# Kernel tuning notes

Measured on AMD Instinct MI355X. Metric: run time of the kernel, lower is better.

Reference implementation:

```python
import jax, jax.numpy as jnp
import numpy as np

# Static sensor configuration (from init_kwargs)
WIDTH = 1024
HEIGHT = 1024
X0, Y0 = -1.0, -1.0
DX = (1.0 - (-1.0)) / WIDTH
DY = (1.0 - (-1.0)) / HEIGHT
SIGMA = 0.1
KERNEL_SIZE = 2

_off = np.arange(-KERNEL_SIZE, KERNEL_SIZE + 1)
_ox, _oy = np.meshgrid(_off, _off, indexing='xy')
OFF_X = jnp.asarray(_ox.flatten(), dtype=jnp.int32)  # [(2k+1)^2] = [25]
OFF_Y = jnp.asarray(_oy.flatten(), dtype=jnp.int32)

N_POINTS = 2_000_000


def setup_inputs() -> dict:
    key = jax.random.key(0)
    k1, k2, k3 = jax.random.split(key, 3)
    x = jax.random.uniform(k1, (N_POINTS,), dtype=jnp.float32)       # in [0,1) subset of bounds
    y = jax.random.uniform(k2, (N_POINTS,), dtype=jnp.float32)
    values = jax.random.normal(k3, (N_POINTS,), dtype=jnp.float32)
    return {"x": x, "y": y, "values": values}


def reference(x, y, values):
    # Map to pixel coordinates
    x_pix = (x - X0) / DX
    y_pix = (y - Y0) / DY
    xi_base = jnp.floor(x_pix).astype(jnp.int32)
    yi_base = jnp.floor(y_pix).astype(jnp.int32)
    x_frac = x_pix - xi_base
    y_frac = y_pix - yi_base

    # [N, 25] neighbor pixel indices and Gaussian weights
    xi = xi_base[:, None] + OFF_X[None, :]
    yi = yi_base[:, None] + OFF_Y[None, :]
    dist_x = x_frac[:, None] - OFF_X[None, :].astype(x_frac.dtype)
    dist_y = y_frac[:, None] - OFF_Y[None, :].astype(y_frac.dtype)
    weights = jnp.exp(-0.5 * (dist_x ** 2 + dist_y ** 2) / (SIGMA ** 2))
    weights = weights / jnp.sum(weights, axis=1, keepdims=True)

    valid = (xi >= 0) & (xi < WIDTH) & (yi >= 0) & (yi < HEIGHT)
    xi = jnp.clip(xi, 0, WIDTH - 1)
    yi = jnp.clip(yi, 0, HEIGHT - 1)

    splatted = values[:, None] * weights * valid  # [N, 25]
    flat_idx = (yi * WIDTH + xi).reshape(-1)      # [N*25]
    img_flat = jax.ops.segment_sum(splatted.reshape(-1), flat_idx,
                                   num_segments=HEIGHT * WIDTH)
    return img_flat.reshape(HEIGHT, WIDTH)
```

## Files before the change

kernel.cpp:

```cpp
#include <hip/hip_runtime.h>
#include <hip/hip_bf16.h>

#define WIDTH 1024
#define HEIGHT 1024
#define IMG_ELEMS (WIDTH * HEIGHT)
#define TPX 32
#define NTILES (TPX * TPX)
#define NB 256
#define BT 1024
#define CAPR 80
#define CAPP 36
#define PTS_CAP 8448

#define OFF_PTS   0
#define OFF_BIDX  (OFF_PTS + 2 * PTS_CAP)
#define OFF_HCNT  (OFF_BIDX + (NTILES * CAPP) / 2)
#define OFF_RCNT  (OFF_HCNT + NTILES)
#define OFF_RDST  (OFF_RCNT + NB)
#define OFF_STMP  (OFF_RDST + NB)
#define SMEM_U32  (OFF_STMP + NB)


__device__ __forceinline__ void point_geom(float px, float py, int& cxb, int& cyb,
                                           float& ax, float& ay) {
    float xp = (px + 1.0f) * 512.0f;
    float yp = (py + 1.0f) * 512.0f;
    int xb = (int)floorf(xp);
    int yb = (int)floorf(yp);
    float xf = xp - (float)xb;
    float yf = yp - (float)yb;
    ax = 1.0f / (1.0f + __expf(100.0f * xf - 50.0f));
    ay = 1.0f / (1.0f + __expf(100.0f * yf - 50.0f));
    cxb = min(max(xb, 0), WIDTH - 1);
    cyb = min(max(yb, 0), HEIGHT - 1);
}

__device__ __forceinline__ void splat_one(float px, float py, float val,
                                          unsigned* cursor, uint2* payload,
                                          unsigned bbase) {
    int cxb, cyb; float ax, ay;
    point_geom(px, py, cxb, cyb, ax, ay);
    int tile = (cyb >> 5) * TPX + (cxb >> 5);
    unsigned pos = atomicAdd(&cursor[tile], 1u);
    if (pos < CAPR) {
        unsigned axq = (unsigned)(ax * 2047.0f + 0.5f);
        unsigned ayq = (unsigned)(ay * 2047.0f + 0.5f);
        unsigned packed = axq | (ayq << 11) |
                          ((unsigned)(cxb & 31) << 22) | ((unsigned)(cyb & 31) << 27);
        payload[(size_t)(bbase | (unsigned)tile) * CAPR + pos] =
            make_uint2(__float_as_uint(val), packed);
    }
}

__global__ void __launch_bounds__(BT)
k_sortlocal(const float* __restrict__ x, const float* __restrict__ y,
            const float* __restrict__ v, uint2* __restrict__ payload,
            unsigned* __restrict__ runCnt, float4* __restrict__ outv,
            int n, int ppb) {
    __shared__ unsigned cursor[NTILES];
    int b = blockIdx.x;
    cursor[threadIdx.x] = 0u;
    outv[(unsigned)b * 1024u + threadIdx.x] = make_float4(0.f, 0.f, 0.f, 0.f);
    __syncthreads();
    int lo = b * ppb;
    int hi = min(n, lo + ppb);
    unsigned bbase = (unsigned)(b << 10);
    for (int base = lo + (int)threadIdx.x * 4; base < hi; base += BT * 4) {
        if (base + 3 < hi) {
            float4 x4 = *(const float4*)&x[base];
            float4 y4 = *(const float4*)&y[base];
            float4 v4 = *(const float4*)&v[base];
            splat_one(x4.x, y4.x, v4.x, cursor, payload, bbase);
            splat_one(x4.y, y4.y, v4.y, cursor, payload, bbase);
            splat_one(x4.z, y4.z, v4.z, cursor, payload, bbase);
            splat_one(x4.w, y4.w, v4.w, cursor, payload, bbase);
        } else {
            for (int i = base; i < hi; ++i)
                splat_one(x[i], y[i], v[i], cursor, payload, bbase);
        }
    }
    __syncthreads();
    runCnt[(unsigned)b * NTILES + threadIdx.x] = min(cursor[threadIdx.x], (unsigned)CAPR);
}

__global__ void __launch_bounds__(BT)
k_accum(const uint2* __restrict__ payload, const unsigned* __restrict__ runCnt,
        float* __restrict__ out) {
    __shared__ unsigned smem[SMEM_U32];
    uint2*          pts  = (uint2*)&smem[OFF_PTS];
    unsigned short* bidx = (unsigned short*)&smem[OFF_BIDX];
    unsigned*       hcnt = &smem[OFF_HCNT];
    unsigned*       rcnt = &smem[OFF_RCNT];
    unsigned*       rdst = &smem[OFF_RDST];
    unsigned*       stmp = &smem[OFF_STMP];
    float*          exT01 = (float*)&smem[OFF_PTS];
    float*          exT11 = (float*)&smem[OFF_PTS + BT];

    unsigned b = blockIdx.x;
    unsigned t;
    if (b < 256u) {
        t = (16u + (b >> 4)) * 32u + 16u + (b & 15u);
    } else {
        unsigned r = b - 256u;
        if (r < 512u) t = r;
        else { unsigned q = r - 512u; t = (16u + (q >> 4)) * 32u + (q & 15u); }
    }

    int p = threadIdx.x;
    unsigned lane = p & 63, w = p >> 6;
    unsigned c0 = 0u;
    if (p < NB) { c0 = runCnt[(unsigned)p * NTILES + t]; rcnt[p] = c0; }
    hcnt[p] = 0u;
    unsigned tsum = c0;
#pragma unroll
    for (int d = 32; d >= 1; d >>= 1) tsum += __shfl_down(tsum, d, 64);
    if (p < NB && lane == 0) rdst[w] = tsum;
    __syncthreads();
    unsigned total = rdst[0] + rdst[1] + rdst[2] + rdst[3];
    if (total == 0) return;

    unsigned vsc = c0;
#pragma unroll
    for (int d = 1; d < 64; d <<= 1) {
        unsigned tmp = __shfl_up(vsc, d, 64);
        if (lane >= (unsigned)d) vsc += tmp;
    }
    __syncthreads();
    if (p < NB && lane == 63) stmp[w] = vsc;
    __syncthreads();
    if (p == 0) {
        unsigned a = 0;
#pragma unroll
        for (int k = 0; k < 4; ++k) { unsigned tt = stmp[k]; stmp[k] = a; a += tt; }
    }
    __syncthreads();
    if (p < NB) rdst[p] = vsc - c0 + stmp[w];
    __syncthreads();

    for (int k = 0; k < 16; ++k) {
        int r = (int)w * 16 + k;
        unsigned cnt = rcnt[r], dst = rdst[r];
        const unsigned long long* g =
            (const unsigned long long*)(payload + (size_t)((unsigned)(r << 10) | t) * CAPR);
        for (unsigned j = lane; j < cnt; j += 64) {
            unsigned long long raw = __builtin_nontemporal_load(&g[j]);
            uint2 pl = make_uint2((unsigned)raw, (unsigned)(raw >> 32));
            unsigned slot = dst + j;
            if (slot < PTS_CAP) {
                pts[slot] = pl;
                unsigned pix = (pl.y >> 22) & 1023u;
                unsigned pos = atomicAdd(&hcnt[pix], 1u);
                if (pos < CAPP) bidx[pix * CAPP + pos] = (unsigned short)slot;
            }
        }
    }
    __syncthreads();

    float t00 = 0.0f, t10 = 0.0f, t01 = 0.0f, t11 = 0.0f;
    unsigned cnt = min(hcnt[p], (unsigned)CAPP);
    for (unsigned e = 0; e < cnt; ++e) {
        uint2 sp = pts[bidx[p * CAPP + e]];
        float val = __uint_as_float(sp.x);
        float ax = (float)(sp.y & 2047u) * (1.0f / 2047.0f);
        float ay = (float)((sp.y >> 11) & 2047u) * (1.0f / 2047.0f);
        float bx = 1.0f - ax, by = 1.0f - ay;
        t00 += val * ax * ay;
        t10 += val * bx * ay;
        t01 += val * ax * by;
        t11 += val * bx * by;
    }
    __syncthreads();
    exT01[p] = t01;
    exT11[p] = t11;
    __syncthreads();

    int lx = p & 31, ly = p >> 5;
    int gx = (int)((t & 31u) << 5) + lx;
    int gy = (int)((t >> 5) << 5) + ly;
    size_t g = (size_t)gy * WIDTH + gx;
    float t10l = __shfl_up(t10, 1, 64);
    float sum = t00;
    if (lx > 0) sum += t10l;
    if (ly > 0) sum += exT01[p - 32];
    if (lx > 0 && ly > 0) sum += exT11[p - 33];
    if (lx == 0 || ly == 0) atomicAdd(&out[g], sum);
    else out[g] = sum;

    bool xr = (gx + 1 < WIDTH), yd = (gy + 1 < HEIGHT);
    if (lx == 31 && xr) {
        atomicAdd(&out[g + 1], t10);
        if (yd) atomicAdd(&out[g + WIDTH + 1], t11);
    }
    if (ly == 31 && yd) {
        atomicAdd(&out[g + WIDTH], t01);
        if (lx < 31 && xr) atomicAdd(&out[g + WIDTH + 1], t11);
    }
}

__global__ void __launch_bounds__(256)
splat_direct(const float* __restrict__ x, const float* __restrict__ y,
             const float* __restrict__ v, float* __restrict__ out, int n) {
    int i = blockIdx.x * blockDim.x + threadIdx.x;
    if (i >= n) return;
    int cxb, cyb; float ax, ay;
    point_geom(x[i], y[i], cxb, cyb, ax, ay);
    float val = v[i];
    float bx = 1.0f - ax, by = 1.0f - ay;
    float* row = out + cyb * WIDTH;
    atomicAdd(row + cxb, val * ax * ay);
    if (cxb + 1 < WIDTH) atomicAdd(row + cxb + 1, val * bx * ay);
    if (cyb + 1 < HEIGHT) {
        row += WIDTH;
        atomicAdd(row + cxb, val * ax * by);
        if (cxb + 1 < WIDTH) atomicAdd(row + cxb + 1, val * bx * by);
    }
}

extern "C" void kernel_launch(void* const* d_in, const int* in_sizes, int n_in,
                              void* d_out, int out_size, void* d_ws, size_t ws_size,
                              hipStream_t stream) {
    const float* x = (const float*)d_in[0];
    const float* y = (const float*)d_in[1];
    const float* v = (const float*)d_in[2];
    float* out = (float*)d_out;
    int n = in_sizes[0];
    int ppb = ((n + NB - 1) / NB + 7) & ~7;

    size_t off_payload = 0;
    size_t off_runcnt  = off_payload + (size_t)NB * NTILES * CAPR * sizeof(uint2);
    size_t need        = off_runcnt + (size_t)NB * NTILES * sizeof(unsigned);
    bool caps_ok = (ppb <= 8192) && (out_size == IMG_ELEMS);

    if (ws_size >= need && caps_ok) {
        char* ws = (char*)d_ws;
        uint2*    payload = (uint2*)(ws + off_payload);
        unsigned* runCnt  = (unsigned*)(ws + off_runcnt);

        k_sortlocal<<<NB, BT, 0, stream>>>(x, y, v, payload, runCnt,
                                           (float4*)out, n, ppb);
        k_accum<<<NTILES, BT, 0, stream>>>(payload, runCnt, out);
    } else {
        (void)hipMemsetAsync(out, 0, (size_t)out_size * sizeof(float), stream);
        splat_direct<<<(n + 255) / 256, 256, 0, stream>>>(x, y, v, out, n);
    }
}
```

Before: 101.2 us.

## Stage bucketed payload in LDS and write compact per-block runs coalesced

The binning kernel no longer scatters each point straight to a fixed-capacity global slot per (block, tile). Each block now counting-sorts its points into shared memory, computing per-tile offsets with a block-wide scan, and writes the packed sorted buffer to global memory with coalesced 16-byte stores. It stores offset and count together in runCnt, and the accumulation kernel reads runs at those offsets using 8 lanes per run. This removes scattered 8-byte global writes and shrinks the payload footprint. It assumes at most 8 points per thread (ppb ≤ 8192), drops the per-tile capacity clamp, and uses 64KB+ of LDS per block.

```diff
diff --git a/kernel.cpp b/kernel.cpp
--- a/kernel.cpp
+++ b/kernel.cpp
@@ -8,7 +8,7 @@
 #define NTILES (TPX * TPX)
 #define NB 256
 #define BT 1024
-#define CAPR 80
+#define BSTRIDE 8192
 #define CAPP 36
 #define PTS_CAP 8448
 
@@ -17,7 +17,8 @@
 #define OFF_HCNT  (OFF_BIDX + (NTILES * CAPP) / 2)
 #define OFF_RCNT  (OFF_HCNT + NTILES)
 #define OFF_RDST  (OFF_RCNT + NB)
-#define OFF_STMP  (OFF_RDST + NB)
+#define OFF_ROFF  (OFF_RDST + NB)
+#define OFF_STMP  (OFF_ROFF + NB)
 #define SMEM_U32  (OFF_STMP + NB)
 
 
@@ -35,52 +36,95 @@
     cyb = min(max(yb, 0), HEIGHT - 1);
 }
 
-__device__ __forceinline__ void splat_one(float px, float py, float val,
-                                          unsigned* cursor, uint2* payload,
-                                          unsigned bbase) {
-    int cxb, cyb; float ax, ay;
-    point_geom(px, py, cxb, cyb, ax, ay);
-    int tile = (cyb >> 5) * TPX + (cxb >> 5);
-    unsigned pos = atomicAdd(&cursor[tile], 1u);
-    if (pos < CAPR) {
-        unsigned axq = (unsigned)(ax * 2047.0f + 0.5f);
-        unsigned ayq = (unsigned)(ay * 2047.0f + 0.5f);
-        unsigned packed = axq | (ayq << 11) |
-                          ((unsigned)(cxb & 31) << 22) | ((unsigned)(cyb & 31) << 27);
-        payload[(size_t)(bbase | (unsigned)tile) * CAPR + pos] =
-            make_uint2(__float_as_uint(val), packed);
-    }
-}
-
 __global__ void __launch_bounds__(BT)
 k_sortlocal(const float* __restrict__ x, const float* __restrict__ y,
             const float* __restrict__ v, uint2* __restrict__ payload,
             unsigned* __restrict__ runCnt, float4* __restrict__ outv,
             int n, int ppb) {
     __shared__ unsigned cursor[NTILES];
+    __shared__ unsigned wtot[BT / 64];
+    __shared__ __align__(16) uint2 stage[BSTRIDE];
+
     int b = blockIdx.x;
-    cursor[threadIdx.x] = 0u;
-    outv[(unsigned)b * 1024u + threadIdx.x] = make_float4(0.f, 0.f, 0.f, 0.f);
-    __syncthreads();
+    int p = threadIdx.x;
+    cursor[p] = 0u;
+    outv[(unsigned)b * 1024u + p] = make_float4(0.f, 0.f, 0.f, 0.f);
+    __syncthreads();
+
     int lo = b * ppb;
     int hi = min(n, lo + ppb);
-    unsigned bbase = (unsigned)(b << 10);
-    for (int base = lo + (int)threadIdx.x * 4; base < hi; base += BT * 4) {
+
+    uint2 pay[8];
+    unsigned meta[8];
+
+    auto enc = [&](int s, float px, float py, float pv) {
+        int cxb, cyb; float ax, ay;
+        point_geom(px, py, cxb, cyb, ax, ay);
+        unsigned tile = (unsigned)((cyb >> 5) * TPX + (cxb >> 5));
+        unsigned pos = atomicAdd(&cursor[tile], 1u);
+        unsigned axq = (unsigned)(ax * 2047.0f + 0.5f);
+        unsigned ayq = (unsigned)(ay * 2047.0f + 0.5f);
+        pay[s] = make_uint2(__float_as_uint(pv),
+                            axq | (ayq << 11) | ((unsigned)(cxb & 31) << 22) |
+                            ((unsigned)(cyb & 31) << 27));
+        meta[s] = (tile << 16) | pos;
+    };
+
+#pragma unroll
+    for (int it = 0; it < 2; ++it) {
+        int base = lo + p * 4 + it * (BT * 4);
         if (base + 3 < hi) {
             float4 x4 = *(const float4*)&x[base];
             float4 y4 = *(const float4*)&y[base];
             float4 v4 = *(const float4*)&v[base];
-            splat_one(x4.x, y4.x, v4.x, cursor, payload, bbase);
-            splat_one(x4.y, y4.y, v4.y, cursor, payload, bbase);
-            splat_one(x4.z, y4.z, v4.z, cursor, payload, bbase);
-            splat_one(x4.w, y4.w, v4.w, cursor, payload, bbase);
+            enc(it * 4 + 0, x4.x, y4.x, v4.x);
+            enc(it * 4 + 1, x4.y, y4.y, v4.y);
+            enc(it * 4 + 2, x4.z, y4.z, v4.z);
+            enc(it * 4 + 3, x4.w, y4.w, v4.w);
         } else {
-            for (int i = base; i < hi; ++i)
-                splat_one(x[i], y[i], v[i], cursor, payload, bbase);
+#pragma unroll
+            for (int j = 0; j < 4; ++j) {
+                int idx = base + j;
+                if (idx < hi) enc(it * 4 + j, x[idx], y[idx], v[idx]);
+                else          meta[it * 4 + j] = 0xFFFFFFFFu;
+            }
         }
     }
     __syncthreads();
-    runCnt[(unsigned)b * NTILES + threadIdx.x] = min(cursor[threadIdx.x], (unsigned)CAPR);
+
+    unsigned c = cursor[p];
+    unsigned lane = p & 63, w = p >> 6;
+    unsigned vsc = c;
+#pragma unroll
+    for (int d = 1; d < 64; d <<= 1) {
+        unsigned t_ = __shfl_up(vsc, d, 64);
+        if (lane >= (unsigned)d) vsc += t_;
+    }
+    if (lane == 63) wtot[w] = vsc;
+    __syncthreads();
+    if (p == 0) {
+        unsigned a = 0;
+#pragma unroll
+        for (int k = 0; k < BT / 64; ++k) { unsigned t_ = wtot[k]; wtot[k] = a; a += t_; }
+    }
+    __syncthreads();
+    unsigned excl = vsc - c + wtot[w];
+    runCnt[(unsigned)b * NTILES + p] = (excl << 16) | c;
+    cursor[p] = excl;
+    __syncthreads();
+
+#pragma unroll
+    for (int s = 0; s < 8; ++s) {
+        unsigned m = meta[s];
+        if (m != 0xFFFFFFFFu)
+            stage[cursor[m >> 16] + (m & 0xFFFFu)] = pay[s];
+    }
+    __syncthreads();
+
+    int nv = ppb >> 1;
+    uint4* dstv = (uint4*)(payload + ((size_t)b << 13));
+    const uint4* srcv = (const uint4*)stage;
+    for (int i = p; i < nv; i += BT) dstv[i] = srcv[i];
 }
 
 __global__ void __launch_bounds__(BT)
@@ -92,6 +136,7 @@
     unsigned*       hcnt = &smem[OFF_HCNT];
     unsigned*       rcnt = &smem[OFF_RCNT];
     unsigned*       rdst = &smem[OFF_RDST];
+    unsigned*       roff = &smem[OFF_ROFF];
     unsigned*       stmp = &smem[OFF_STMP];
     float*          exT01 = (float*)&smem[OFF_PTS];
     float*          exT11 = (float*)&smem[OFF_PTS + BT];
@@ -109,7 +154,12 @@
     int p = threadIdx.x;
     unsigned lane = p & 63, w = p >> 6;
     unsigned c0 = 0u;
-    if (p < NB) { c0 = runCnt[(unsigned)p * NTILES + t]; rcnt[p] = c0; }
+    if (p < NB) {
+        unsigned pk = runCnt[(unsigned)p * NTILES + t];
+        c0 = pk & 0xFFFFu;
+        rcnt[p] = c0;
+        roff[p] = pk >> 16;
+    }
     hcnt[p] = 0u;
     unsigned tsum = c0;
 #pragma unroll
@@ -137,12 +187,14 @@
     if (p < NB) rdst[p] = vsc - c0 + stmp[w];
     __syncthreads();
 
-    for (int k = 0; k < 16; ++k) {
-        int r = (int)w * 16 + k;
+    unsigned sub = lane >> 3, jl = lane & 7u;
+#pragma unroll
+    for (int kk = 0; kk < 2; ++kk) {
+        int r = (int)w * 16 + kk * 8 + (int)sub;
         unsigned cnt = rcnt[r], dst = rdst[r];
         const unsigned long long* g =
-            (const unsigned long long*)(payload + (size_t)((unsigned)(r << 10) | t) * CAPR);
-        for (unsigned j = lane; j < cnt; j += 64) {
+            (const unsigned long long*)(payload + (((size_t)r) << 13) + roff[r]);
+        for (unsigned j = jl; j < cnt; j += 8) {
             unsigned long long raw = __builtin_nontemporal_load(&g[j]);
             uint2 pl = make_uint2((unsigned)raw, (unsigned)(raw >> 32));
             unsigned slot = dst + j;
@@ -227,9 +279,9 @@
     int ppb = ((n + NB - 1) / NB + 7) & ~7;
 
     size_t off_payload = 0;
-    size_t off_runcnt  = off_payload + (size_t)NB * NTILES * CAPR * sizeof(uint2);
+    size_t off_runcnt  = off_payload + (size_t)NB * BSTRIDE * sizeof(uint2);
     size_t need        = off_runcnt + (size_t)NB * NTILES * sizeof(unsigned);
-    bool caps_ok = (ppb <= 8192) && (out_size == IMG_ELEMS);
+    bool caps_ok = (ppb <= BSTRIDE) && (out_size == IMG_ELEMS);
 
     if (ws_size >= need && caps_ok) {
         char* ws = (char*)d_ws;
```

Result: faster. 95.30 us (-5.9%).
